# Optimization experiments

Measured on AMD Instinct MI355X. Metric: run time of the kernel, lower is better.

The kernel has to match this reference:

```python
import jax, jax.numpy as jnp
import numpy as np

D_MODEL = 256
N_HEADS = 8
D_HEAD = D_MODEL // N_HEADS
EMB = [16, 16, 16, 16]
CUMSUM = [0, 16, 32, 48, 64]
PSUM = sum(EMB)
LEVELS = [(122, 122), (61, 61), (31, 31), (16, 16)]
S_TOTAL = sum(h * w for h, w in LEVELS)
IMG = 976.0


def swap_pairs(x):
    # swap consecutive pairs along the leading (view) dim
    return x.reshape(-1, 2, *x.shape[1:])[:, ::-1].reshape(x.shape)


def grid_sample_bilinear(img, grid):
    # img: [B, H, W, D]; grid: [B, Q, 2] in [-1, 1]; align_corners=False, zero padding
    B, H, W, D = img.shape
    gx = (grid[..., 0] + 1.0) * (W * 0.5) - 0.5
    gy = (grid[..., 1] + 1.0) * (H * 0.5) - 0.5
    x0 = jnp.floor(gx)
    y0 = jnp.floor(gy)
    wx = (gx - x0)[..., None]
    wy = (gy - y0)[..., None]
    x0i = x0.astype(jnp.int32)
    y0i = y0.astype(jnp.int32)
    flat = img.reshape(B, H * W, D)

    def gather(xi, yi):
        valid = ((xi >= 0) & (xi < W) & (yi >= 0) & (yi < H)).astype(img.dtype)
        idx = jnp.clip(yi, 0, H - 1) * W + jnp.clip(xi, 0, W - 1)
        v = jnp.take_along_axis(flat, idx[..., None], axis=1)
        return v * valid[..., None]

    v00 = gather(x0i, y0i)
    v01 = gather(x0i + 1, y0i)
    v10 = gather(x0i, y0i + 1)
    v11 = gather(x0i + 1, y0i + 1)
    return (v00 * (1 - wx) * (1 - wy) + v01 * wx * (1 - wy)
            + v10 * (1 - wx) * wy + v11 * wx * wy)


def ms_deform_attn_core(value, shapes, sampling_locations, attention_weights):
    # value: [N, S, M, D]; sampling_locations: [N, Lq, M, P, 2]; attention_weights: [N, Lq, M, P]
    N, S, M, D = value.shape
    Lq = sampling_locations.shape[1]
    grids = 2.0 * sampling_locations - 1.0
    outs = []
    start = 0
    for lid, (H, W) in enumerate(shapes):
        p0, p1 = CUMSUM[lid], CUMSUM[lid + 1]
        Pl = p1 - p0
        v = value[:, start:start + H * W].reshape(N, H, W, M, D)
        v = v.transpose(0, 3, 1, 2, 4).reshape(N * M, H, W, D)
        g = grids[:, :, :, p0:p1].transpose(0, 2, 1, 3, 4).reshape(N * M, Lq * Pl, 2)
        outs.append(grid_sample_bilinear(v, g).reshape(N * M, Lq, Pl, D))
        start += H * W
    samp = jnp.concatenate(outs, axis=2)  # [N*M, Lq, Psum, D]
    w = attention_weights.transpose(0, 2, 1, 3).reshape(N * M, Lq, PSUM, 1)
    out = (samp * w).sum(axis=2)  # [N*M, Lq, D]
    return out.reshape(N, M, Lq, D).transpose(0, 2, 1, 3).reshape(N, Lq, M * D)


def _forward(query, input_flatten, reference_points, p_pfws, pt_transforms,
             W_val, b_val, W_attn, b_attn, W_out, b_out, shapes):
    N, Lq, _ = query.shape
    value = (input_flatten @ W_val.T + b_val).reshape(N, -1, N_HEADS, D_HEAD)
    attn = jax.nn.softmax((query @ W_attn.T + b_attn).reshape(N, Lq, N_HEADS, PSUM), axis=-1)

    # reverse 2x3 affine transform on reference points, scale to pixels
    A = pt_transforms[:, :, :2]
    t = pt_transforms[:, :, 2]
    orig = jnp.einsum('nij,nqj->nqi', jnp.linalg.inv(A), reference_points - t[:, None, :]) * IMG

    # epipolar line in the second (swapped) view: point(x) = ts + ms * x, x in [0, IMG]
    P1 = p_pfws
    P2 = swap_pairs(p_pfws)
    A1 = P1[:, :, :3]
    b1 = P1[:, :, 3]
    cam = -jnp.linalg.solve(A1, b1[:, :, None])[:, :, 0]  # camera center [N,3]
    uh = jnp.concatenate([orig, jnp.ones_like(orig[..., :1])], -1)
    ray = jnp.einsum('nij,nqj->nqi', jnp.linalg.inv(A1), uh - b1[:, None, :])  # [N,Q,3]

    def proj2(X):
        Xh = jnp.concatenate([X, jnp.ones_like(X[..., :1])], -1)
        y = jnp.einsum('nij,nqj->nqi', P2, Xh)
        return y[..., :2] / (y[..., 2:3] + 1e-8)

    ts = proj2(jnp.broadcast_to(cam[:, None, :], ray.shape))
    ms = (proj2(ray) - ts) / IMG

    locs = []
    for n_pts in EMB:
        xs = jnp.linspace(0.0, IMG, n_pts)
        locs.append(ts[:, :, None, :] + ms[:, :, None, :] * xs[None, None, :, None])
    loc = jnp.concatenate(locs, axis=2) / IMG  # [N, Lq, Psum, 2]

    T2 = swap_pairs(pt_transforms)
    loc = jnp.einsum('nij,nqpj->nqpi', T2[:, :, :2], loc) + T2[:, :, 2][:, None, None, :]
    loc = jnp.clip(loc, 0.0, 1.0)
    samp_loc = jnp.broadcast_to(loc[:, :, None, :, :], (N, Lq, N_HEADS, PSUM, 2))

    out = ms_deform_attn_core(swap_pairs(value), shapes, samp_loc, attn)
    return out @ W_out.T + b_out


def setup_inputs() -> dict:
    key = jax.random.key(0)
    ks = jax.random.split(key, 12)
    N, Lq = 4, 1000
    query = jax.random.normal(ks[0], (N, Lq, D_MODEL), jnp.float32)
    input_flatten = jax.random.normal(ks[1], (N, S_TOTAL, D_MODEL), jnp.float32)
    reference_points = jax.random.uniform(ks[2], (N, Lq, 2), jnp.float32)
    p_pfws = jnp.asarray(np.eye(3, 4), jnp.float32) + 0.05 * jax.random.normal(ks[3], (N, 3, 4), jnp.float32)
    pt_transforms = jnp.asarray(np.eye(2, 3), jnp.float32) + 0.05 * jax.random.normal(ks[4], (N, 2, 3), jnp.float32)
    W_val = 0.05 * jax.random.normal(ks[5], (D_MODEL, D_MODEL), jnp.float32)
    b_val = jnp.zeros((D_MODEL,), jnp.float32)
    W_attn = 0.05 * jax.random.normal(ks[6], (N_HEADS * PSUM, D_MODEL), jnp.float32)
    b_attn = jnp.zeros((N_HEADS * PSUM,), jnp.float32)
    W_out = 0.05 * jax.random.normal(ks[7], (D_MODEL, D_MODEL), jnp.float32)
    b_out = jnp.zeros((D_MODEL,), jnp.float32)
    input_spatial_shapes = np.asarray(LEVELS, np.int64)
    input_level_start_index = np.asarray(np.cumsum([0] + [h * w for h, w in LEVELS])[:-1], np.int64)
    return {"query": query, "input_flatten": input_flatten, "reference_points": reference_points,
            "p_pfws": p_pfws, "pt_transforms": pt_transforms,
            "W_val": W_val, "b_val": b_val, "W_attn": W_attn, "b_attn": b_attn,
            "W_out": W_out, "b_out": b_out,
            "input_spatial_shapes": input_spatial_shapes,
            "input_level_start_index": input_level_start_index}


def reference(query, input_flatten, reference_points, p_pfws, pt_transforms,
              W_val, b_val, W_attn, b_attn, W_out, b_out,
              input_spatial_shapes, input_level_start_index):
    shapes = [(int(h), int(w)) for h, w in np.asarray(input_spatial_shapes)]
    return _forward(query, input_flatten, reference_points, p_pfws, pt_transforms,
                    W_val, b_val, W_attn, b_attn, W_out, b_out, shapes)
```

## Files before the change

kernel.cpp:

```cpp
#include <hip/hip_runtime.h>
#include <hip/hip_bf16.h>
#include <math.h>

#define NB 4
#define LQ 1000
#define NHEAD 8
#define DHEAD 32
#define DMODEL 256
#define PSUM 64
#define STOT 19822
#define IMGF 976.0f
#define GK 256

__device__ __constant__ int c_LH[4] = {122, 61, 31, 16};
__device__ __constant__ int c_LW[4] = {122, 61, 31, 16};
__device__ __constant__ int c_LST[4] = {0, 14884, 18605, 19566};

typedef __attribute__((ext_vector_type(8))) short bf16x8;
typedef __attribute__((ext_vector_type(4))) float f32x4;

__device__ inline unsigned int pk2(float a, float b) {
    unsigned short ua = __bfloat16_as_ushort(__float2bfloat16(a));
    unsigned short ub = __bfloat16_as_ushort(__float2bfloat16(b));
    return (unsigned int)ua | ((unsigned int)ub << 16);
}
__device__ inline float bf2f(unsigned short u) {
    return __uint_as_float(((unsigned int)u) << 16);
}
__device__ inline void gll16(const void* g, void* l) {
    __builtin_amdgcn_global_load_lds(
        (const __attribute__((address_space(1))) void*)g,
        (__attribute__((address_space(3))) void*)l, 16, 0, 0);
}

__device__ inline void make_consts(int n, const float* p_pfws, const float* pt,
                                   float* consts) {
    const float* P1 = p_pfws + n * 12;
    const float* P2 = p_pfws + (n ^ 1) * 12;
    const float* T  = pt + n * 6;
    const float* T2 = pt + (n ^ 1) * 6;
    float* C = consts + n * 48;
    float det = T[0]*T[4] - T[1]*T[3];
    float idet = 1.0f/det;
    C[0] =  T[4]*idet; C[1] = -T[1]*idet;
    C[2] = -T[3]*idet; C[3] =  T[0]*idet;
    C[4] = T[2]; C[5] = T[5];
    float a=P1[0], b=P1[1], c=P1[2];
    float d=P1[4], e=P1[5], f=P1[6];
    float g=P1[8], h=P1[9], i=P1[10];
    float b10=P1[3], b11=P1[7], b12=P1[11];
    float A_=e*i-f*h, B_=c*h-b*i, Cc=b*f-c*e;
    float D_=f*g-d*i, E_=a*i-c*g, F_=c*d-a*f;
    float G_=d*h-e*g, H_=b*g-a*h, I_=a*e-b*d;
    float det3 = a*A_ + b*D_ + c*G_;
    float id3 = 1.0f/det3;
    C[6]=A_*id3;  C[7]=B_*id3;  C[8]=Cc*id3;
    C[9]=D_*id3;  C[10]=E_*id3; C[11]=F_*id3;
    C[12]=G_*id3; C[13]=H_*id3; C[14]=I_*id3;
    C[15]=b10; C[16]=b11; C[17]=b12;
    for (int k = 0; k < 12; ++k) C[18+k] = P2[k];
    float cam0 = -(C[6]*b10  + C[7]*b11  + C[8]*b12);
    float cam1 = -(C[9]*b10  + C[10]*b11 + C[11]*b12);
    float cam2 = -(C[12]*b10 + C[13]*b11 + C[14]*b12);
    float y0 = P2[0]*cam0 + P2[1]*cam1 + P2[2]*cam2  + P2[3];
    float y1 = P2[4]*cam0 + P2[5]*cam1 + P2[6]*cam2  + P2[7];
    float y2 = P2[8]*cam0 + P2[9]*cam1 + P2[10]*cam2 + P2[11];
    float inv = 1.0f/(y2 + 1e-8f);
    C[30] = y0*inv; C[31] = y1*inv;
    for (int k = 0; k < 6; ++k) C[32+k] = T2[k];
}

__global__ void prep(const float* __restrict__ Wv, const float* __restrict__ Wa,
                     const float* __restrict__ Wo,
                     unsigned short* __restrict__ wbv, unsigned short* __restrict__ wba,
                     unsigned short* __restrict__ wbo,
                     const float* __restrict__ p_pfws, const float* __restrict__ pt,
                     float* __restrict__ consts) {
    int bid = blockIdx.x;
    if (bid == 256) {
        int n = threadIdx.x;
        if (n < NB) make_consts(n, p_pfws, pt, consts);
        return;
    }
    int i = bid * 256 + threadIdx.x;
    const float* src; unsigned short* dst; int off;
    if (i < 16384)      { src = Wv; dst = wbv; off = i; }
    else if (i < 49152) { src = Wa; dst = wba; off = i - 16384; }
    else                { src = Wo; dst = wbo; off = i - 49152; }
    float4 f = ((const float4*)src)[off];
    ushort4 o;
    o.x = __bfloat16_as_ushort(__float2bfloat16(f.x));
    o.y = __bfloat16_as_ushort(__float2bfloat16(f.y));
    o.z = __bfloat16_as_ushort(__float2bfloat16(f.z));
    o.w = __bfloat16_as_ushort(__float2bfloat16(f.w));
    ((ushort4*)dst)[off] = o;
}

template<bool OUT_BF16>
__global__ __launch_bounds__(256, 4)
void gemm64(const float* __restrict__ A, const unsigned short* __restrict__ Bb,
            const float* __restrict__ bias, void* __restrict__ outp,
            int M, int N) {
    __shared__ char smem[40960];
    char* asmem = smem;
    char* bsmem = smem + 8192;
    const int tid  = threadIdx.x;
    const int lane = tid & 63;
    const int w    = tid >> 6;
    const int l15  = lane & 15;
    const int koct = lane >> 4;
    const int i0 = blockIdx.x * 64;
    const int o0 = blockIdx.y * 256;

    const int s_row = tid >> 2;
    const int s_q   = tid & 3;
    int gr = i0 + s_row; gr = gr < M ? gr : M - 1;
    const float* aptr = A + (size_t)gr * GK + s_q * 16;
    const int s_sw = (s_row & 7) << 4;
    char* a_w0 = asmem + s_row * 128 + ((s_q * 32)      ^ s_sw);
    char* a_w1 = asmem + s_row * 128 + ((s_q * 32 + 16) ^ s_sw);

    const int b_sub = lane >> 3;
    const int b_kc  = (lane & 7) ^ b_sub;

    f32x4 acc[4][4] = {};
    float bias_v[4];
    #pragma unroll
    for (int ni = 0; ni < 4; ++ni) bias_v[ni] = bias[o0 + w * 64 + ni * 16 + l15];

    for (int t = 0; t < 4; ++t) {
        const int k0 = t * 64;
        #pragma unroll
        for (int j = 0; j < 8; ++j) {
            int cI = w * 8 + j;
            int col = cI * 8 + b_sub;
            gll16(Bb + (size_t)(o0 + col) * GK + k0 + b_kc * 8,
                  bsmem + cI * 1024);
        }
        {
            const float4* s = (const float4*)(aptr + k0);
            float4 f0 = s[0], f1 = s[1], f2 = s[2], f3 = s[3];
            uint4 wv0, wv1;
            wv0.x = pk2(f0.x,f0.y); wv0.y = pk2(f0.z,f0.w);
            wv0.z = pk2(f1.x,f1.y); wv0.w = pk2(f1.z,f1.w);
            wv1.x = pk2(f2.x,f2.y); wv1.y = pk2(f2.z,f2.w);
            wv1.z = pk2(f3.x,f3.y); wv1.w = pk2(f3.z,f3.w);
            *(uint4*)a_w0 = wv0;
            *(uint4*)a_w1 = wv1;
        }
        __syncthreads();
        #pragma unroll
        for (int ks = 0; ks < 2; ++ks) {
            const int kc = ks * 4 + koct;
            bf16x8 af[4], bfr[4];
            #pragma unroll
            for (int mi = 0; mi < 4; ++mi) {
                int r = mi * 16 + l15;
                af[mi] = *(const bf16x8*)(asmem + r * 128 + ((kc * 16) ^ ((r & 7) << 4)));
            }
            #pragma unroll
            for (int ni = 0; ni < 4; ++ni) {
                int c = w * 64 + ni * 16 + l15;
                bfr[ni] = *(const bf16x8*)(bsmem + c * 128 + ((kc * 16) ^ ((c & 7) << 4)));
            }
            #pragma unroll
            for (int mi = 0; mi < 4; ++mi)
                #pragma unroll
                for (int ni = 0; ni < 4; ++ni)
                    acc[mi][ni] = __builtin_amdgcn_mfma_f32_16x16x32_bf16(
                        af[mi], bfr[ni], acc[mi][ni], 0, 0, 0);
        }
        __syncthreads();
    }

    if (OUT_BF16) {
        #pragma unroll
        for (int mi = 0; mi < 4; ++mi)
            #pragma unroll
            for (int j = 0; j < 4; ++j) {
                int r = mi * 16 + (lane >> 4) * 4 + j;
                #pragma unroll
                for (int ni = 0; ni < 4; ++ni) {
                    int c = w * 64 + ni * 16 + l15;
                    float v = acc[mi][ni][j] + bias_v[ni];
                    *(unsigned short*)(smem + r * 512 + c * 2) =
                        __bfloat16_as_ushort(__float2bfloat16(v));
                }
            }
        __syncthreads();
        int r = tid >> 2, q = tid & 3;
        int grow = i0 + r;
        if (grow < M) {
            const uint4* src = (const uint4*)(smem + r * 512 + q * 128);
            uint4* dst = (uint4*)((unsigned short*)outp + (size_t)grow * N + o0 + q * 64);
            #pragma unroll
            for (int i = 0; i < 8; ++i) dst[i] = src[i];
        }
    } else {
        #pragma unroll
        for (int mi = 0; mi < 4; ++mi) {
            int rbase = i0 + mi * 16 + (lane >> 4) * 4;
            #pragma unroll
            for (int j = 0; j < 4; ++j) {
                int grow = rbase + j;
                if (grow < M) {
                    #pragma unroll
                    for (int ni = 0; ni < 4; ++ni) {
                        int gcol = o0 + w * 64 + ni * 16 + l15;
                        ((float*)outp)[(size_t)grow * N + gcol] = acc[mi][ni][j] + bias_v[ni];
                    }
                }
            }
        }
    }
}

__global__ __launch_bounds__(256)
void fused_sample(const float* __restrict__ logits,
                  const float* __restrict__ ref_pts,
                  const unsigned short* __restrict__ value,
                  const float* __restrict__ consts,
                  float* __restrict__ attn_out) {
    int b = blockIdx.x;
    int n = b / LQ;
    int q = b - n * LQ;
    int tid = threadIdx.x;

    __shared__ float s_attn[512];
    __shared__ float s_loc[16][2];
    __shared__ int   s_idx[64][4];
    __shared__ float s_w[64][4];
    __shared__ float4 s_part[4][64];

    s_attn[tid]       = logits[(size_t)b * 512 + tid];
    s_attn[tid + 256] = logits[(size_t)b * 512 + tid + 256];
    __syncthreads();

    {
        int wave = tid >> 6, lane = tid & 63;
        for (int h = wave; h < NHEAD; h += 4) {
            float v = s_attn[h * 64 + lane];
            float mx = v;
            #pragma unroll
            for (int off = 32; off; off >>= 1) mx = fmaxf(mx, __shfl_xor(mx, off, 64));
            float e = expf(v - mx);
            float sm = e;
            #pragma unroll
            for (int off = 32; off; off >>= 1) sm += __shfl_xor(sm, off, 64);
            s_attn[h * 64 + lane] = e / sm;
        }
    }

    if (tid < 16) {
        const float* C = consts + n * 48;
        float rx = ref_pts[((size_t)n * LQ + q) * 2 + 0];
        float ry = ref_pts[((size_t)n * LQ + q) * 2 + 1];
        float dx = rx - C[4], dy = ry - C[5];
        float ox = (C[0]*dx + C[1]*dy) * IMGF;
        float oy = (C[2]*dx + C[3]*dy) * IMGF;
        float u0 = ox - C[15], u1 = oy - C[16], u2 = 1.0f - C[17];
        float r0 = C[6]*u0  + C[7]*u1  + C[8]*u2;
        float r1 = C[9]*u0  + C[10]*u1 + C[11]*u2;
        float r2 = C[12]*u0 + C[13]*u1 + C[14]*u2;
        float y0 = C[18]*r0 + C[19]*r1 + C[20]*r2 + C[21];
        float y1 = C[22]*r0 + C[23]*r1 + C[24]*r2 + C[25];
        float y2 = C[26]*r0 + C[27]*r1 + C[28]*r2 + C[29];
        float inv = 1.0f/(y2 + 1e-8f);
        float prx = y0*inv, pry = y1*inv;
        float ts0 = C[30], ts1 = C[31];
        float msx = (prx - ts0) / IMGF, msy = (pry - ts1) / IMGF;
        int j = tid;
        float xsj = IMGF * ((float)j / 15.0f);
        float lx = (ts0 + msx * xsj) / IMGF;
        float ly = (ts1 + msy * xsj) / IMGF;
        float Lx = C[32]*lx + C[33]*ly + C[34];
        float Ly = C[35]*lx + C[36]*ly + C[37];
        s_loc[j][0] = fminf(fmaxf(Lx, 0.0f), 1.0f);
        s_loc[j][1] = fminf(fmaxf(Ly, 0.0f), 1.0f);
    }
    __syncthreads();

    if (tid < 64) {
        int p = tid, lev = p >> 4, j = p & 15;
        int H = c_LH[lev], W = c_LW[lev], st = c_LST[lev];
        float gx = s_loc[j][0] * (float)W - 0.5f;
        float gy = s_loc[j][1] * (float)H - 0.5f;
        float x0f = floorf(gx), y0f = floorf(gy);
        float wx = gx - x0f, wy = gy - y0f;
        int x0 = (int)x0f, y0 = (int)y0f;
        int x1 = x0 + 1, y1 = y0 + 1;
        bool vx0 = (x0 >= 0) & (x0 < W), vx1 = (x1 >= 0) & (x1 < W);
        bool vy0 = (y0 >= 0) & (y0 < H), vy1 = (y1 >= 0) & (y1 < H);
        s_idx[p][0] = (vx0 & vy0) ? st + y0 * W + x0 : -1;  s_w[p][0] = (1.f-wx)*(1.f-wy);
        s_idx[p][1] = (vx1 & vy0) ? st + y0 * W + x1 : -1;  s_w[p][1] = wx*(1.f-wy);
        s_idx[p][2] = (vx0 & vy1) ? st + y1 * W + x0 : -1;  s_w[p][2] = (1.f-wx)*wy;
        s_idx[p][3] = (vx1 & vy1) ? st + y1 * W + x1 : -1;  s_w[p][3] = wx*wy;
    }
    __syncthreads();

    int wv = tid >> 6, lane = tid & 63;
    const unsigned short* vbase = value + (size_t)(n ^ 1) * STOT * DMODEL + lane * 4;
    int m = lane >> 3;
    float a0 = 0.f, a1 = 0.f, a2 = 0.f, a3 = 0.f;
    #pragma unroll 4
    for (int j = 0; j < 16; ++j) {
        int p = wv * 16 + j;
        float wa = s_attn[m * 64 + p];
        float s0 = 0.f, s1 = 0.f, s2 = 0.f, s3 = 0.f;
        #pragma unroll
        for (int cc = 0; cc < 4; ++cc) {
            int idx = s_idx[p][cc];
            if (idx >= 0) {
                ushort4 vv = *(const ushort4*)(vbase + (size_t)idx * DMODEL);
                float wgt = s_w[p][cc];
                s0 += wgt * bf2f(vv.x);
                s1 += wgt * bf2f(vv.y);
                s2 += wgt * bf2f(vv.z);
                s3 += wgt * bf2f(vv.w);
            }
        }
        a0 += wa * s0; a1 += wa * s1; a2 += wa * s2; a3 += wa * s3;
    }
    s_part[wv][lane] = make_float4(a0, a1, a2, a3);
    __syncthreads();

    const float* sp = (const float*)s_part;
    float r = sp[tid] + sp[256 + tid] + sp[512 + tid] + sp[768 + tid];
    attn_out[(size_t)b * DMODEL + tid] = r;
}

extern "C" void kernel_launch(void* const* d_in, const int* in_sizes, int n_in,
                              void* d_out, int out_size, void* d_ws, size_t ws_size,
                              hipStream_t stream) {
    const float* query         = (const float*)d_in[0];
    const float* input_flatten = (const float*)d_in[1];
    const float* ref_pts       = (const float*)d_in[2];
    const float* p_pfws        = (const float*)d_in[3];
    const float* pt            = (const float*)d_in[4];
    const float* W_val         = (const float*)d_in[5];
    const float* b_val         = (const float*)d_in[6];
    const float* W_attn        = (const float*)d_in[7];
    const float* b_attn        = (const float*)d_in[8];
    const float* W_out         = (const float*)d_in[9];
    const float* b_out         = (const float*)d_in[10];
    float* out = (float*)d_out;

    const int M = NB * STOT;
    const size_t value_bytes  = (size_t)M * DMODEL * 2;
    const size_t logits_bytes = (size_t)NB * LQ * 512 * 4;
    const size_t attn_bytes   = (size_t)NB * LQ * DMODEL * 4;
    const size_t consts_bytes = NB * 48 * 4;
    const size_t wv_bytes     = (size_t)DMODEL * DMODEL * 2;
    const size_t wa_bytes     = (size_t)512 * DMODEL * 2;
    const size_t wo_bytes     = (size_t)DMODEL * DMODEL * 2;
    const size_t need = value_bytes + logits_bytes + attn_bytes + consts_bytes
                      + wv_bytes + wa_bytes + wo_bytes;
    if (ws_size < need) return;

    char* p = (char*)d_ws;
    unsigned short* value = (unsigned short*)p;  p += value_bytes;
    float* logits   = (float*)p;                 p += logits_bytes;
    float* attn_out = (float*)p;                 p += attn_bytes;
    float* consts   = (float*)p;                 p += consts_bytes;
    unsigned short* wb_val  = (unsigned short*)p; p += wv_bytes;
    unsigned short* wb_attn = (unsigned short*)p; p += wa_bytes;
    unsigned short* wb_out  = (unsigned short*)p; p += wo_bytes;

    prep<<<257, 256, 0, stream>>>(W_val, W_attn, W_out, wb_val, wb_attn, wb_out,
                                  p_pfws, pt, consts);

    {
        dim3 g((M + 63) / 64, 1);
        gemm64<true><<<g, 256, 0, stream>>>(input_flatten, wb_val, b_val, value, M, DMODEL);
    }
    {
        dim3 g((NB * LQ + 63) / 64, 2);
        gemm64<false><<<g, 256, 0, stream>>>(query, wb_attn, b_attn, logits, NB * LQ, 512);
    }
    fused_sample<<<NB * LQ, 256, 0, stream>>>(logits, ref_pts, value, consts, attn_out);
    {
        dim3 g((NB * LQ + 63) / 64, 1);
        gemm64<false><<<g, 256, 0, stream>>>(attn_out, wb_out, b_out, out, NB * LQ, DMODEL);
    }
}
```

Baseline: 99.99 us.

## Add persistent value-projection GEMM keeping weight slice resident in LDS

The value projection GEMM is replaced with a persistent-style kernel. Each block loads a 128-column slice of the bf16 weights into LDS once, then walks ten 32-row tiles of the fp32 input, converting them to bf16 in registers. Loads of the next A tile are double-buffered in registers so they overlap the MFMA compute of the current tile. The generic gemm64 bf16 epilogue is also simplified to direct scattered stores instead of staging through LDS. The aim is to cut repeated weight traffic and per-tile launch overhead, at the cost of fewer blocks (about 2 per 10 tiles), less parallelism and uncoalesced 2-byte output stores.

```diff
diff --git a/kernel.cpp b/kernel.cpp
--- a/kernel.cpp
+++ b/kernel.cpp
@@ -26,6 +26,12 @@
 }
 __device__ inline float bf2f(unsigned short u) {
     return __uint_as_float(((unsigned int)u) << 16);
+}
+__device__ inline bf16x8 cvt8(float4 u, float4 v) {
+    union { unsigned int w[4]; bf16x8 h; } r;
+    r.w[0] = pk2(u.x, u.y); r.w[1] = pk2(u.z, u.w);
+    r.w[2] = pk2(v.x, v.y); r.w[3] = pk2(v.z, v.w);
+    return r.h;
 }
 __device__ inline void gll16(const void* g, void* l) {
     __builtin_amdgcn_global_load_lds(
@@ -96,6 +102,124 @@
     ((ushort4*)dst)[off] = o;
 }
 
+__global__ __launch_bounds__(256, 2)
+void gemm_val_persist(const float* __restrict__ X, const unsigned short* __restrict__ Wb,
+                      const float* __restrict__ bias, unsigned short* __restrict__ out,
+                      int M, int T) {
+    __shared__ __align__(16) unsigned short Bs[128 * 256];
+    __shared__ __align__(16) unsigned short As[32 * 256];
+    const int bid  = blockIdx.x;
+    const int rgrp = bid >> 1, half = bid & 1;
+    const int c0   = half * 128;
+    const int t0   = rgrp * 10;
+    int nt = T - t0; if (nt > 10) nt = 10;
+    if (nt <= 0) return;
+    const int tid  = threadIdx.x;
+    const int lane = tid & 63;
+    const int w    = tid >> 6;
+    const int wr   = w >> 1, wc = w & 1;
+    const int l15  = lane & 15;
+    const int koct = lane >> 4;
+
+    #pragma unroll
+    for (int j = 0; j < 16; ++j) {
+        int e    = (w * 16 + j) * 64 + lane;
+        int colp = e >> 5;
+        int chp  = e & 31;
+        int chl  = chp ^ (colp & 7);
+        gll16(Wb + ((size_t)(c0 + colp)) * GK + chl * 8,
+              (char*)Bs + colp * 512 + chp * 16);
+    }
+
+    const int srow = tid >> 3;
+    const int sch  = tid & 7;
+    float4 rA[8], rB[8];
+
+#define LOADA(R, t) do {                                                        \
+        int _r = (t) * 32 + srow; if (_r >= M) _r = M - 1;                      \
+        const float* _p = X + (size_t)_r * GK;                                  \
+        _Pragma("unroll") for (int _c = 0; _c < 4; ++_c) {                      \
+            R[_c*2]   = *(const float4*)(_p + (sch + 8*_c) * 8);                \
+            R[_c*2+1] = *(const float4*)(_p + (sch + 8*_c) * 8 + 4);            \
+        } } while (0)
+
+#define WRITEA(R) do {                                                          \
+        _Pragma("unroll") for (int _c = 0; _c < 4; ++_c) {                      \
+            int _ch = sch + 8*_c;                                               \
+            bf16x8 _v = cvt8(R[_c*2], R[_c*2+1]);                               \
+            *(bf16x8*)((char*)As + srow * 512 + ((_ch ^ (srow & 7)) * 16)) = _v;\
+        } } while (0)
+
+    float bias_v[4];
+    #pragma unroll
+    for (int ni = 0; ni < 4; ++ni) bias_v[ni] = bias[c0 + wc * 64 + ni * 16 + l15];
+
+    LOADA(rA, t0);
+    if (nt > 1) LOADA(rB, t0 + 1);
+    asm volatile("s_waitcnt vmcnt(0)" ::: "memory");
+    WRITEA(rA);
+    asm volatile("s_waitcnt lgkmcnt(0)" ::: "memory");
+    __builtin_amdgcn_s_barrier();
+    asm volatile("" ::: "memory");
+
+#define COMPUTE_STORE(I) do {                                                   \
+        f32x4 acc[4] = {};                                                      \
+        const int _row = wr * 16 + l15;                                         \
+        const int _asw = (_row & 7);                                            \
+        _Pragma("unroll") for (int ks = 0; ks < 8; ++ks) {                      \
+            int _ch = ks * 4 + koct;                                            \
+            bf16x8 af = *(const bf16x8*)((char*)As + _row * 512 +               \
+                                         ((_ch ^ _asw) * 16));                  \
+            _Pragma("unroll") for (int ni = 0; ni < 4; ++ni) {                  \
+                int _col = wc * 64 + ni * 16 + l15;                             \
+                bf16x8 bfr = *(const bf16x8*)((char*)Bs + _col * 512 +          \
+                                              ((_ch ^ (_col & 7)) * 16));       \
+                acc[ni] = __builtin_amdgcn_mfma_f32_16x16x32_bf16(              \
+                    af, bfr, acc[ni], 0, 0, 0);                                 \
+            }                                                                   \
+        }                                                                       \
+        int _rb = (t0 + (I)) * 32 + wr * 16 + (lane >> 4) * 4;                  \
+        _Pragma("unroll") for (int _j = 0; _j < 4; ++_j) {                      \
+            int _gr = _rb + _j;                                                 \
+            if (_gr < M) {                                                      \
+                _Pragma("unroll") for (int ni = 0; ni < 4; ++ni) {              \
+                    int _gc = c0 + wc * 64 + ni * 16 + l15;                     \
+                    out[(size_t)_gr * DMODEL + _gc] = __bfloat16_as_ushort(     \
+                        __float2bfloat16(acc[ni][_j] + bias_v[ni]));            \
+                }                                                               \
+            }                                                                   \
+        } } while (0)
+
+    int i = 0;
+    while (true) {
+        COMPUTE_STORE(i);
+        asm volatile("" ::: "memory");
+        __builtin_amdgcn_s_barrier();
+        asm volatile("" ::: "memory");
+        if (i + 1 >= nt) break;
+        if (i + 2 < nt) LOADA(rA, t0 + i + 2);
+        WRITEA(rB);
+        asm volatile("s_waitcnt lgkmcnt(0)" ::: "memory");
+        __builtin_amdgcn_s_barrier();
+        asm volatile("" ::: "memory");
+
+        COMPUTE_STORE(i + 1);
+        asm volatile("" ::: "memory");
+        __builtin_amdgcn_s_barrier();
+        asm volatile("" ::: "memory");
+        if (i + 2 >= nt) break;
+        if (i + 3 < nt) LOADA(rB, t0 + i + 3);
+        WRITEA(rA);
+        asm volatile("s_waitcnt lgkmcnt(0)" ::: "memory");
+        __builtin_amdgcn_s_barrier();
+        asm volatile("" ::: "memory");
+        i += 2;
+    }
+#undef COMPUTE_STORE
+#undef WRITEA
+#undef LOADA
+}
+
 template<bool OUT_BF16>
 __global__ __launch_bounds__(256, 4)
 void gemm64(const float* __restrict__ A, const unsigned short* __restrict__ Bb,
@@ -173,42 +297,22 @@
         __syncthreads();
     }
 
-    if (OUT_BF16) {
+    #pragma unroll
+    for (int mi = 0; mi < 4; ++mi) {
+        int rbase = i0 + mi * 16 + (lane >> 4) * 4;
         #pragma unroll
-        for (int mi = 0; mi < 4; ++mi)
-            #pragma unroll
-            for (int j = 0; j < 4; ++j) {
-                int r = mi * 16 + (lane >> 4) * 4 + j;
+        for (int j = 0; j < 4; ++j) {
+            int grow = rbase + j;
+            if (grow < M) {
                 #pragma unroll
                 for (int ni = 0; ni < 4; ++ni) {
-                    int c = w * 64 + ni * 16 + l15;
+                    int gcol = o0 + w * 64 + ni * 16 + l15;
                     float v = acc[mi][ni][j] + bias_v[ni];
-                    *(unsigned short*)(smem + r * 512 + c * 2) =
-                        __bfloat16_as_ushort(__float2bfloat16(v));
-                }
-            }
-        __syncthreads();
-        int r = tid >> 2, q = tid & 3;
-        int grow = i0 + r;
-        if (grow < M) {
-            const uint4* src = (const uint4*)(smem + r * 512 + q * 128);
-            uint4* dst = (uint4*)((unsigned short*)outp + (size_t)grow * N + o0 + q * 64);
-            #pragma unroll
-            for (int i = 0; i < 8; ++i) dst[i] = src[i];
-        }
-    } else {
-        #pragma unroll
-        for (int mi = 0; mi < 4; ++mi) {
-            int rbase = i0 + mi * 16 + (lane >> 4) * 4;
-            #pragma unroll
-            for (int j = 0; j < 4; ++j) {
-                int grow = rbase + j;
-                if (grow < M) {
-                    #pragma unroll
-                    for (int ni = 0; ni < 4; ++ni) {
-                        int gcol = o0 + w * 64 + ni * 16 + l15;
-                        ((float*)outp)[(size_t)grow * N + gcol] = acc[mi][ni][j] + bias_v[ni];
-                    }
+                    if (OUT_BF16)
+                        ((unsigned short*)outp)[(size_t)grow * N + gcol] =
+                            __bfloat16_as_ushort(__float2bfloat16(v));
+                    else
+                        ((float*)outp)[(size_t)grow * N + gcol] = v;
                 }
             }
         }
@@ -370,8 +474,10 @@
                                   p_pfws, pt, consts);
 
     {
-        dim3 g((M + 63) / 64, 1);
-        gemm64<true><<<g, 256, 0, stream>>>(input_flatten, wb_val, b_val, value, M, DMODEL);
+        const int T = (M + 31) / 32;
+        const int ngrp = (T + 9) / 10;
+        gemm_val_persist<<<ngrp * 2, 256, 0, stream>>>(input_flatten, wb_val, b_val,
+                                                       value, M, T);
     }
     {
         dim3 g((NB * LQ + 63) / 64, 2);
```

Result: faster. 97.27 us (-2.7%).

## Add register-resident-weight value projection GEMM with double-buffered LDS row staging

Applied to the files above, without the earlier changes.

Replaces the value-projection GEMM with a new kernel that keeps the full bf16 weight slice for each wave in registers. The kernel streams 32-row fp32 input tiles through double-buffered LDS using async global-to-LDS loads, with explicit vmcnt waits and barriers, and converts the inputs to bf16 just before the MFMA. Each block walks a chunk of five tiles, so the weight loads are amortized and input loads overlap compute. The generic gemm64 bf16 output path also drops its LDS-staged coalesced store in favour of direct scalar stores, which may reduce write efficiency for the remaining bf16 users. The register-held weights raise register pressure, limiting occupancy to about two blocks per CU.

```diff
diff --git a/kernel.cpp b/kernel.cpp
--- a/kernel.cpp
+++ b/kernel.cpp
@@ -27,10 +27,23 @@
 __device__ inline float bf2f(unsigned short u) {
     return __uint_as_float(((unsigned int)u) << 16);
 }
+__device__ inline bf16x8 cvt8(float4 u, float4 v) {
+    union { unsigned int w[4]; bf16x8 h; } r;
+    r.w[0] = pk2(u.x, u.y); r.w[1] = pk2(u.z, u.w);
+    r.w[2] = pk2(v.x, v.y); r.w[3] = pk2(v.z, v.w);
+    return r.h;
+}
 __device__ inline void gll16(const void* g, void* l) {
     __builtin_amdgcn_global_load_lds(
         (const __attribute__((address_space(1))) void*)g,
         (__attribute__((address_space(3))) void*)l, 16, 0, 0);
+}
+__device__ inline void hard_barrier() {
+    asm volatile("" ::: "memory");
+    __builtin_amdgcn_sched_barrier(0);
+    __builtin_amdgcn_s_barrier();
+    __builtin_amdgcn_sched_barrier(0);
+    asm volatile("" ::: "memory");
 }
 
 __device__ inline void make_consts(int n, const float* p_pfws, const float* pt,
@@ -96,6 +109,91 @@
     ((ushort4*)dst)[off] = o;
 }
 
+__global__ __launch_bounds__(256, 2)
+void gemm_val_regB(const float* __restrict__ X, const unsigned short* __restrict__ Wb,
+                   const float* __restrict__ bias, unsigned short* __restrict__ out,
+                   int M, int T, int CHUNK) {
+    __shared__ __align__(16) char As[2][32768];
+    const int tid  = threadIdx.x;
+    const int lane = tid & 63;
+    const int wq   = tid >> 6;
+    const int l15  = lane & 15;
+    const int koct = lane >> 4;
+    const int t0   = blockIdx.x * CHUNK;
+    int nt = T - t0; if (nt > CHUNK) nt = CHUNK;
+    if (nt <= 0) return;
+
+    bf16x8 breg[8][4];
+    #pragma unroll
+    for (int ks = 0; ks < 8; ++ks)
+        #pragma unroll
+        for (int ni = 0; ni < 4; ++ni) {
+            int col = wq * 64 + ni * 16 + l15;
+            breg[ks][ni] = *(const bf16x8*)((const char*)Wb + (size_t)col * 512
+                                            + ks * 64 + koct * 16);
+        }
+    float bias_v[4];
+    #pragma unroll
+    for (int ni = 0; ni < 4; ++ni) bias_v[ni] = bias[wq * 64 + ni * 16 + l15];
+
+#define STAGE(g, b) do {                                                      \
+        _Pragma("unroll") for (int j = 0; j < 8; ++j) {                       \
+            int r_ = wq * 8 + j;                                              \
+            int gr_ = (g) * 32 + r_; if (gr_ >= M) gr_ = M - 1;               \
+            int lch_ = lane ^ (r_ & 7);                                       \
+            gll16(X + (size_t)gr_ * GK + lch_ * 4, As[b] + r_ * 1024);        \
+        } } while (0)
+
+    STAGE(t0, 0);
+    if (nt > 1) { STAGE(t0 + 1, 1); asm volatile("s_waitcnt vmcnt(8)" ::: "memory"); }
+    else        {                   asm volatile("s_waitcnt vmcnt(0)" ::: "memory"); }
+    hard_barrier();
+
+#define COMPUTE_STORE(g, b) do {                                              \
+        f32x4 acc[2][4] = {};                                                 \
+        _Pragma("unroll") for (int ks = 0; ks < 8; ++ks) {                    \
+            _Pragma("unroll") for (int mi = 0; mi < 2; ++mi) {                \
+                int r_ = mi * 16 + l15;                                       \
+                int ch_ = ks * 8 + koct * 2;                                  \
+                float4 x0_ = *(const float4*)(As[b] + r_ * 1024 +             \
+                                              ((ch_    ) ^ (r_ & 7)) * 16);   \
+                float4 x1_ = *(const float4*)(As[b] + r_ * 1024 +             \
+                                              ((ch_ + 1) ^ (r_ & 7)) * 16);   \
+                bf16x8 af_ = cvt8(x0_, x1_);                                  \
+                _Pragma("unroll") for (int ni = 0; ni < 4; ++ni)              \
+                    acc[mi][ni] = __builtin_amdgcn_mfma_f32_16x16x32_bf16(    \
+                        af_, breg[ks][ni], acc[mi][ni], 0, 0, 0);             \
+            }                                                                 \
+        }                                                                     \
+        _Pragma("unroll") for (int mi = 0; mi < 2; ++mi) {                    \
+            int rb_ = (g) * 32 + mi * 16 + (lane >> 4) * 4;                   \
+            _Pragma("unroll") for (int j_ = 0; j_ < 4; ++j_) {                \
+                int gr_ = rb_ + j_;                                           \
+                if (gr_ < M) {                                                \
+                    _Pragma("unroll") for (int ni = 0; ni < 4; ++ni)          \
+                        out[(size_t)gr_ * DMODEL + wq * 64 + ni * 16 + l15] = \
+                            __bfloat16_as_ushort(__float2bfloat16(            \
+                                acc[mi][ni][j_] + bias_v[ni]));               \
+                }                                                             \
+            }                                                                 \
+        } } while (0)
+
+    for (int t = 0; t < nt; ++t) {
+        COMPUTE_STORE(t0 + t, t & 1);
+        if (t + 1 == nt) break;
+        hard_barrier();
+        if (t + 2 < nt) {
+            STAGE(t0 + t + 2, t & 1);
+            asm volatile("s_waitcnt vmcnt(8)" ::: "memory");
+        } else {
+            asm volatile("s_waitcnt vmcnt(0)" ::: "memory");
+        }
+        hard_barrier();
+    }
+#undef COMPUTE_STORE
+#undef STAGE
+}
+
 template<bool OUT_BF16>
 __global__ __launch_bounds__(256, 4)
 void gemm64(const float* __restrict__ A, const unsigned short* __restrict__ Bb,
@@ -173,42 +271,22 @@
         __syncthreads();
     }
 
-    if (OUT_BF16) {
+    #pragma unroll
+    for (int mi = 0; mi < 4; ++mi) {
+        int rbase = i0 + mi * 16 + (lane >> 4) * 4;
         #pragma unroll
-        for (int mi = 0; mi < 4; ++mi)
-            #pragma unroll
-            for (int j = 0; j < 4; ++j) {
-                int r = mi * 16 + (lane >> 4) * 4 + j;
+        for (int j = 0; j < 4; ++j) {
+            int grow = rbase + j;
+            if (grow < M) {
                 #pragma unroll
                 for (int ni = 0; ni < 4; ++ni) {
-                    int c = w * 64 + ni * 16 + l15;
+                    int gcol = o0 + w * 64 + ni * 16 + l15;
                     float v = acc[mi][ni][j] + bias_v[ni];
-                    *(unsigned short*)(smem + r * 512 + c * 2) =
-                        __bfloat16_as_ushort(__float2bfloat16(v));
-                }
-            }
-        __syncthreads();
-        int r = tid >> 2, q = tid & 3;
-        int grow = i0 + r;
-        if (grow < M) {
-            const uint4* src = (const uint4*)(smem + r * 512 + q * 128);
-            uint4* dst = (uint4*)((unsigned short*)outp + (size_t)grow * N + o0 + q * 64);
-            #pragma unroll
-            for (int i = 0; i < 8; ++i) dst[i] = src[i];
-        }
-    } else {
-        #pragma unroll
-        for (int mi = 0; mi < 4; ++mi) {
-            int rbase = i0 + mi * 16 + (lane >> 4) * 4;
-            #pragma unroll
-            for (int j = 0; j < 4; ++j) {
-                int grow = rbase + j;
-                if (grow < M) {
-                    #pragma unroll
-                    for (int ni = 0; ni < 4; ++ni) {
-                        int gcol = o0 + w * 64 + ni * 16 + l15;
-                        ((float*)outp)[(size_t)grow * N + gcol] = acc[mi][ni][j] + bias_v[ni];
-                    }
+                    if (OUT_BF16)
+                        ((unsigned short*)outp)[(size_t)grow * N + gcol] =
+                            __bfloat16_as_ushort(__float2bfloat16(v));
+                    else
+                        ((float*)outp)[(size_t)grow * N + gcol] = v;
                 }
             }
         }
@@ -370,8 +448,11 @@
                                   p_pfws, pt, consts);
 
     {
-        dim3 g((M + 63) / 64, 1);
-        gemm64<true><<<g, 256, 0, stream>>>(input_flatten, wb_val, b_val, value, M, DMODEL);
+        const int T = (M + 31) / 32;
+        const int CHUNK = 5;
+        const int blocks = (T + CHUNK - 1) / CHUNK;
+        gemm_val_regB<<<blocks, 256, 0, stream>>>(input_flatten, wb_val, b_val,
+                                                  value, M, T, CHUNK);
     }
     {
         dim3 g((NB * LQ + 63) / 64, 2);
```

Result: faster. 96.29 us (-3.7%).
